# Optimization experiments

Measured on AMD Instinct MI355X. Metric: run time of the kernel, lower is better.

Reference implementation:

```python
import jax, jax.numpy as jnp
import numpy as np

B, S, H = 16, 4096, 768
N_SENT = 32
HH = H // 2  # per-direction LSTM hidden
NUM_LAYERS = 2


def attn_pool(x, mask, Wp, bp, v):
    # x: [N, L, H]; torch Linear is x @ W.T + b
    scores = jnp.einsum('nlh,h->nl', jnp.tanh(jnp.einsum('nlh,gh->nlg', x, Wp) + bp), v)
    if mask is not None:
        scores = jnp.where(mask, scores, -jnp.inf)
    w = jax.nn.softmax(scores, axis=1)  # [N, L]
    pooled = jnp.einsum('nlh,nl->nh', x, w)
    return pooled, w


def lstm_dir(x, Wih, Whh, bih, bhh, reverse):
    # x: [B, T, In]; PyTorch gate order i, f, g, o
    xg = jnp.einsum('bti,gi->btg', x, Wih) + bih  # [B, T, 4*HH]
    Bn = x.shape[0]
    init = (jnp.zeros((Bn, HH), x.dtype), jnp.zeros((Bn, HH), x.dtype))

    def step(carry, xt):
        h, c = carry
        g = xt + jnp.einsum('bh,gh->bg', h, Whh) + bhh
        i, f, gg, o = jnp.split(g, 4, axis=-1)
        c = jax.nn.sigmoid(f) * c + jax.nn.sigmoid(i) * jnp.tanh(gg)
        h = jax.nn.sigmoid(o) * jnp.tanh(c)
        return (h, c), h

    _, hs = jax.lax.scan(step, init, jnp.swapaxes(xg, 0, 1), reverse=reverse)
    return jnp.swapaxes(hs, 0, 1)  # [B, T, HH], time-aligned


def bilstm(x, Wih, Whh, bih, bhh):
    h = x
    for l in range(NUM_LAYERS):
        f = lstm_dir(h, Wih[l, 0], Whh[l, 0], bih[l, 0], bhh[l, 0], False)
        b = lstm_dir(h, Wih[l, 1], Whh[l, 1], bih[l, 1], bhh[l, 1], True)
        h = jnp.concatenate([f, b], axis=-1)  # [B, T, H]
    return h


def setup_inputs() -> dict:
    key = jax.random.key(0)
    ks = jax.random.split(key, 12)
    std = 0.02
    return {
        'hidden_states': jax.random.normal(ks[0], (B, S, H), jnp.float32),
        'attention_mask': jnp.ones((B, S), jnp.bool_),
        'w_proj_w': jax.random.normal(ks[1], (H, H), jnp.float32) * std,
        'w_proj_b': jnp.zeros((H,), jnp.float32),
        'w_vec': jax.random.normal(ks[2], (H,), jnp.float32) * std,
        'lstm_Wih': jax.random.normal(ks[3], (NUM_LAYERS, 2, 4 * HH, H), jnp.float32) * std,
        'lstm_Whh': jax.random.normal(ks[4], (NUM_LAYERS, 2, 4 * HH, HH), jnp.float32) * std,
        'lstm_bih': jnp.zeros((NUM_LAYERS, 2, 4 * HH), jnp.float32),
        'lstm_bhh': jnp.zeros((NUM_LAYERS, 2, 4 * HH), jnp.float32),
        's_proj_w': jax.random.normal(ks[5], (H, H), jnp.float32) * std,
        's_proj_b': jnp.zeros((H,), jnp.float32),
        's_vec': jax.random.normal(ks[6], (H,), jnp.float32) * std,
        'n_sent': N_SENT,
    }


def reference(hidden_states, attention_mask, w_proj_w, w_proj_b, w_vec,
              lstm_Wih, lstm_Whh, lstm_bih, lstm_bhh,
              s_proj_w, s_proj_b, s_vec, n_sent):
    b, s, h = hidden_states.shape
    L = s // n_sent
    # uniform sentence segmentation (boundaries at k*L-1): vectorized word attention
    x = hidden_states.reshape(b * n_sent, L, h)
    m = attention_mask.reshape(b * n_sent, L)
    pooled, w_attn = attn_pool(x, m, w_proj_w, w_proj_b, w_vec)  # [b*n_sent, h]
    sent = pooled.reshape(b, n_sent, h)
    enc = bilstm(sent, lstm_Wih, lstm_Whh, lstm_bih, lstm_bhh)  # [b, n_sent, h]
    doc, s_attn = attn_pool(enc, None, s_proj_w, s_proj_b, s_vec)  # [b, h]
    return doc, w_attn.reshape(b, n_sent, L), s_attn
```

## Files before the change

kernel.cpp:

```cpp
#include <hip/hip_runtime.h>
#include <math.h>

#define NB     16
#define NSENT  32
#define LW     128
#define HD     768
#define HH     384
#define NG     1536
#define NROWS  (NB*NSENT)
#define MW     (NROWS*LW)

typedef unsigned short ushort_t;
typedef unsigned long long u64;
typedef __attribute__((ext_vector_type(8))) short bf16x8;
typedef __attribute__((ext_vector_type(4))) float f32x4;
typedef __attribute__((ext_vector_type(4))) unsigned short u16x4;
typedef __attribute__((ext_vector_type(4))) unsigned int u32x4;

#define MFMA_BF16(a, b, c) __builtin_amdgcn_mfma_f32_16x16x32_bf16((a), (b), (c), 0, 0, 0)

__device__ __forceinline__ ushort_t f2bf(float x) {
  union { float f; unsigned u; } v; v.f = x;
  unsigned r = v.u + 0x7FFFu + ((v.u >> 16) & 1u);
  return (ushort_t)(r >> 16);
}
__device__ __forceinline__ float bf2f(ushort_t b) {
  union { unsigned u; float f; } v; v.u = ((unsigned)b) << 16; return v.f;
}
__device__ __forceinline__ float tanh_fast(float x) {
  float e = __builtin_amdgcn_exp2f(x * 2.88539008177793f);
  return 1.0f - 2.0f * __builtin_amdgcn_rcpf(e + 1.0f);
}
__device__ __forceinline__ float sigm(float x) {
  float e = __builtin_amdgcn_exp2f(-x * 1.44269504088896f);
  return __builtin_amdgcn_rcpf(1.0f + e);
}
__device__ __forceinline__ bf16x8 cvt8(float4 x, float4 y) {
  union { unsigned u[4]; bf16x8 v; } o;
  asm("v_cvt_pk_bf16_f32 %0, %1, %2" : "=v"(o.u[0]) : "v"(x.x), "v"(x.y));
  asm("v_cvt_pk_bf16_f32 %0, %1, %2" : "=v"(o.u[1]) : "v"(x.z), "v"(x.w));
  asm("v_cvt_pk_bf16_f32 %0, %1, %2" : "=v"(o.u[2]) : "v"(y.x), "v"(y.y));
  asm("v_cvt_pk_bf16_f32 %0, %1, %2" : "=v"(o.u[3]) : "v"(y.z), "v"(y.w));
  return o.v;
}
__device__ __forceinline__ void gload16(const void* g, void* l) {
  __builtin_amdgcn_global_load_lds(
      (const __attribute__((address_space(1))) unsigned int*)g,
      (__attribute__((address_space(3))) unsigned int*)l, 16, 0, 0);
}
__device__ __forceinline__ u64 ld64_ic(const u64* p) {
  return __hip_atomic_load(p, __ATOMIC_RELAXED, __HIP_MEMORY_SCOPE_AGENT);
}
__device__ __forceinline__ void st32_ic(unsigned* p, unsigned v) {
  __hip_atomic_store(p, v, __ATOMIC_RELAXED, __HIP_MEMORY_SCOPE_AGENT);
}
__device__ __forceinline__ bool bad64(u64 v) {
  return ((unsigned)v == 0xFFFFFFFFu) | ((unsigned)(v >> 32) == 0xFFFFFFFFu);
}

__global__ void cvt_kernel(const float* __restrict__ in, ushort_t* __restrict__ out, int n) {
  int i = blockIdx.x * blockDim.x + threadIdx.x;
  int st = gridDim.x * blockDim.x;
  for (; i < n; i += st) out[i] = f2bf(in[i]);
}

__global__ void cvtv_kernel(const float* __restrict__ in, ushort_t* __restrict__ out, int n8) {
  int i = blockIdx.x * blockDim.x + threadIdx.x;
  int st = gridDim.x * blockDim.x;
  for (; i < n8; i += st) {
    const float4* p = (const float4*)(in + (size_t)i * 8);
    float4 a = p[0], b = p[1];
    *(bf16x8*)(out + (size_t)i * 8) = cvt8(a, b);
  }
}

__global__ void addvec_kernel(const float* __restrict__ a, const float* __restrict__ b,
                              float* __restrict__ o, int n) {
  int i = blockIdx.x * blockDim.x + threadIdx.x;
  if (i < n) o[i] = a[i] + b[i];
}

__global__ void fillu_kernel(unsigned* __restrict__ p, unsigned v, int n) {
  int i = blockIdx.x * blockDim.x + threadIdx.x;
  int st = gridDim.x * blockDim.x;
  for (; i < n; i += st) p[i] = v;
}

template<int EPI, int SWZ>
__global__ __launch_bounds__(512, 2) void gemm_kernel(
    const ushort_t* __restrict__ Ab, const ushort_t* __restrict__ W,
    const float* __restrict__ bias, const float* __restrict__ vvec,
    float* __restrict__ outp, int Mtotal, int Ntot)
{
  __shared__ __align__(16) char smem[122880];
  short* Albuf = (short*)smem;
  short* Blbuf = (short*)(smem + 49152);
  float* pbuf  = (float*)smem;

  const int tid = threadIdx.x;
  int nc, m0;
  if constexpr (SWZ == 1) {
    const int g = blockIdx.x;
    const int x = g & 7, s = g >> 3;
    nc = s & 3;
    m0 = (x + 8 * (s >> 2)) * 128;
  } else {
    nc = blockIdx.x;
    m0 = blockIdx.y * 128;
  }
  const int n0 = nc * 192;

  const unsigned wbase = (unsigned)(tid & ~63) * 16;

  const int w = tid >> 6, wr = w >> 2, wc = w & 3;
  const int l = tid & 63, lm = l & 15, lg = l >> 4;
  int arow[4], ar7[4];
  #pragma unroll
  for (int mt = 0; mt < 4; ++mt) { arow[mt] = wr * 64 + mt * 16 + lm; ar7[mt] = arow[mt] & 7; }
  int brow[3], br7[3];
  #pragma unroll
  for (int nt = 0; nt < 3; ++nt) { brow[nt] = wc * 48 + nt * 16 + lm; br7[nt] = brow[nt] & 7; }

  f32x4 acc[4][3];
  #pragma unroll
  for (int mt = 0; mt < 4; ++mt)
    #pragma unroll
    for (int nt = 0; nt < 3; ++nt) acc[mt][nt] = (f32x4){0.f, 0.f, 0.f, 0.f};

  const int a0r = tid >> 3,          a0u = (tid & 7) ^ (a0r & 7);
  const int a1r = (tid + 512) >> 3,  a1u = (tid & 7) ^ (a1r & 7);
  const int b2r = (tid + 1024) >> 3, b2u = (tid & 7) ^ (b2r & 7);

  auto stage = [&](int buf, int s) {
    const int kc = s * 64;
    char* Ad = (char*)Albuf + buf * 16384;
    char* Bd = (char*)Blbuf + buf * 24576;
    gload16(Ab + (size_t)(m0 + a0r) * HD + kc + a0u * 8, Ad + wbase);
    gload16(Ab + (size_t)(m0 + a1r) * HD + kc + a1u * 8, Ad + 8192 + wbase);
    gload16(W + (size_t)(n0 + a0r) * HD + kc + a0u * 8, Bd + wbase);
    gload16(W + (size_t)(n0 + a1r) * HD + kc + a1u * 8, Bd + 8192 + wbase);
    gload16(W + (size_t)(n0 + b2r) * HD + kc + b2u * 8, Bd + 16384 + wbase);
  };
  auto compute = [&](int buf) {
    const short* Asrc = Albuf + buf * 8192;
    const short* Bsrc = Blbuf + buf * 12288;
    #pragma unroll
    for (int kk = 0; kk < 2; ++kk) {
      const int u = kk * 4 + lg;
      bf16x8 af[4], bfr[3];
      #pragma unroll
      for (int mt = 0; mt < 4; ++mt)
        af[mt] = *(const bf16x8*)((const char*)Asrc + (unsigned)((arow[mt] * 8 + (u ^ ar7[mt])) << 4));
      #pragma unroll
      for (int nt = 0; nt < 3; ++nt)
        bfr[nt] = *(const bf16x8*)((const char*)Bsrc + (unsigned)((brow[nt] * 8 + (u ^ br7[nt])) << 4));
      #pragma unroll
      for (int mt = 0; mt < 4; ++mt)
        #pragma unroll
        for (int nt = 0; nt < 3; ++nt)
          acc[mt][nt] = MFMA_BF16(af[mt], bfr[nt], acc[mt][nt]);
    }
  };

  stage(0, 0);
  stage(1, 1);
  #pragma unroll
  for (int s = 0; s < 12; ++s) {
    if (s + 2 < 12) stage((s + 2) % 3, s + 2);
    if (s <= 9)       asm volatile("s_waitcnt vmcnt(10)" ::: "memory");
    else if (s == 10) asm volatile("s_waitcnt vmcnt(5)" ::: "memory");
    else              asm volatile("s_waitcnt vmcnt(0)" ::: "memory");
    __builtin_amdgcn_sched_barrier(0);
    __builtin_amdgcn_s_barrier();
    __builtin_amdgcn_sched_barrier(0);
    compute(s % 3);
    __builtin_amdgcn_sched_barrier(0);
    __builtin_amdgcn_s_barrier();
  }

  if constexpr (EPI == 0) {
    float sp[16];
    #pragma unroll
    for (int e = 0; e < 16; ++e) sp[e] = 0.f;
    #pragma unroll
    for (int nt = 0; nt < 3; ++nt) {
      const int col = n0 + wc * 48 + nt * 16 + lm;
      const float bb = bias[col], vv = vvec[col];
      #pragma unroll
      for (int mt = 0; mt < 4; ++mt)
        #pragma unroll
        for (int r = 0; r < 4; ++r)
          sp[mt * 4 + r] += tanh_fast(acc[mt][nt][r] + bb) * vv;
    }
    #pragma unroll
    for (int msk = 1; msk < 16; msk <<= 1)
      #pragma unroll
      for (int e = 0; e < 16; ++e) sp[e] += __shfl_xor(sp[e], msk, 64);
    if (lm == 0) {
      #pragma unroll
      for (int mt = 0; mt < 4; ++mt)
        #pragma unroll
        for (int r = 0; r < 4; ++r)
          pbuf[(wr * 4 + wc) * 64 + mt * 16 + lg * 4 + r] = sp[mt * 4 + r];
    }
    __syncthreads();
    if (tid < 128) {
      const int wrr = tid >> 6, idx = tid & 63;
      float ssum = pbuf[(wrr * 4 + 0) * 64 + idx] + pbuf[(wrr * 4 + 1) * 64 + idx]
                 + pbuf[(wrr * 4 + 2) * 64 + idx] + pbuf[(wrr * 4 + 3) * 64 + idx];
      outp[(size_t)nc * Mtotal + m0 + wrr * 64 + idx] = ssum;
    }
  } else {
    #pragma unroll
    for (int nt = 0; nt < 3; ++nt) {
      const int col = n0 + wc * 48 + nt * 16 + lm;
      const float bb = bias[col];
      #pragma unroll
      for (int mt = 0; mt < 4; ++mt) {
        const int mrow = m0 + wr * 64 + mt * 16 + lg * 4;
        #pragma unroll
        for (int r = 0; r < 4; ++r)
          outp[(size_t)(mrow + r) * Ntot + col] = acc[mt][nt][r] + bb;
      }
    }
  }
}

__global__ __launch_bounds__(64) void softmax128_kernel(const float* __restrict__ sc,
                                                        float* __restrict__ wout) {
  const int row = blockIdx.x, lane = threadIdx.x;
  float a = sc[row * 128 + lane]          + sc[MW + row * 128 + lane]
          + sc[2 * MW + row * 128 + lane] + sc[3 * MW + row * 128 + lane];
  float b = sc[row * 128 + 64 + lane]          + sc[MW + row * 128 + 64 + lane]
          + sc[2 * MW + row * 128 + 64 + lane] + sc[3 * MW + row * 128 + 64 + lane];
  float mx = fmaxf(a, b);
  #pragma unroll
  for (int m = 1; m < 64; m <<= 1) mx = fmaxf(mx, __shfl_xor(mx, m, 64));
  float ea = __builtin_amdgcn_exp2f((a - mx) * 1.44269504088896f);
  float eb = __builtin_amdgcn_exp2f((b - mx) * 1.44269504088896f);
  float s = ea + eb;
  #pragma unroll
  for (int m = 1; m < 64; m <<= 1) s += __shfl_xor(s, m, 64);
  float inv = 1.0f / s;
  wout[row * 128 + lane] = ea * inv;
  wout[row * 128 + 64 + lane] = eb * inv;
}

__global__ __launch_bounds__(192) void pool_kernel(
    const ushort_t* __restrict__ xbf, const float* __restrict__ wattn,
    ushort_t* __restrict__ pooledbf)
{
  __shared__ float wl[128];
  const int n = blockIdx.x, tid = threadIdx.x;
  if (tid < 128) wl[tid] = wattn[n * 128 + tid];
  __syncthreads();
  const ushort_t* xb = xbf + (size_t)n * LW * HD + tid * 4;
  float a0 = 0, a1 = 0, a2 = 0, a3 = 0;
  float b0 = 0, b1 = 0, b2 = 0, b3 = 0;
  for (int lq = 0; lq < LW; lq += 2) {
    u16x4 v0 = *(const u16x4*)(xb + (size_t)lq * HD);
    u16x4 v1 = *(const u16x4*)(xb + (size_t)(lq + 1) * HD);
    float w0 = wl[lq], w1 = wl[lq + 1];
    a0 += w0 * bf2f(v0[0]); a1 += w0 * bf2f(v0[1]);
    a2 += w0 * bf2f(v0[2]); a3 += w0 * bf2f(v0[3]);
    b0 += w1 * bf2f(v1[0]); b1 += w1 * bf2f(v1[1]);
    b2 += w1 * bf2f(v1[2]); b3 += w1 * bf2f(v1[3]);
  }
  u16x4 o;
  o[0] = f2bf(a0 + b0); o[1] = f2bf(a1 + b1); o[2] = f2bf(a2 + b2); o[3] = f2bf(a3 + b3);
  *(u16x4*)(pooledbf + (size_t)n * HD + tid * 4) = o;
}

__global__ __launch_bounds__(384) void lstm_kernel(
    const ushort_t* __restrict__ whh_l,
    const float* __restrict__ xg,
    unsigned* __restrict__ hb32,
    ushort_t* __restrict__ encbf,
    float* __restrict__ encf,
    int writef32)
{
  __shared__ __align__(16) short h_lds[16 * HH];
  __shared__ float gatebuf[16][100];
  __shared__ float cst[16][24];
  const int tid = threadIdx.x;
  const int d = blockIdx.x >> 4, cid = blockIdx.x & 15;
  const int w = tid >> 6, l = tid & 63, lm = l & 15, lg = l >> 4;
  const int b = tid / 24, jj = tid % 24, gj = cid * 24 + jj;

  bf16x8 wf[12];
  {
    int r = w * 16 + lm;
    int qq = r / 24, jjr = r % 24;
    const ushort_t* src = whh_l + ((size_t)d * NG + qq * HH + cid * 24 + jjr) * HH + lg * 8;
    #pragma unroll
    for (int kk = 0; kk < 12; ++kk) wf[kk] = *(const bf16x8*)(src + kk * 32);
  }
  cst[b][jj] = 0.f;
  __syncthreads();

  const int hr = tid / 24, hc = tid % 24;
  const int hu = hc * 2, hx = hr & 7;

  for (int t = 0; t < NSENT; ++t) {
    const int trev = d ? (NSENT - 1 - t) : t;
    const float* xp = xg + (size_t)(b * NSENT + trev) * 3072 + d * NG + gj;
    float xi = xp[0], xf = xp[HH], xgg = xp[2 * HH], xo = xp[3 * HH];

    f32x4 acc = (f32x4){0.f, 0.f, 0.f, 0.f};
    if (t > 0) {
      const u64* src = (const u64*)hb32 + (size_t)(d * NSENT + (t - 1)) * 1536 + hr * 96 + hc * 4;
      u64 v0, v1, v2, v3;
      for (;;) {
        v0 = ld64_ic(src + 0); v1 = ld64_ic(src + 1);
        v2 = ld64_ic(src + 2); v3 = ld64_ic(src + 3);
        if (!(bad64(v0) | bad64(v1) | bad64(v2) | bad64(v3))) break;
        __builtin_amdgcn_s_sleep(1);
      }
      u32x4 lo = (u32x4){(unsigned)v0, (unsigned)(v0 >> 32), (unsigned)v1, (unsigned)(v1 >> 32)};
      u32x4 hi = (u32x4){(unsigned)v2, (unsigned)(v2 >> 32), (unsigned)v3, (unsigned)(v3 >> 32)};
      *(u32x4*)((char*)h_lds + (unsigned)((hr * 48 + ((hu    ) ^ hx)) * 16)) = lo;
      *(u32x4*)((char*)h_lds + (unsigned)((hr * 48 + ((hu + 1) ^ hx)) * 16)) = hi;
      __syncthreads();

      #pragma unroll
      for (int kk = 0; kk < 12; ++kk) {
        bf16x8 a = *(const bf16x8*)((char*)h_lds +
                      (unsigned)((lm * 48 + ((kk * 4 + lg) ^ (lm & 7))) * 16));
        acc = MFMA_BF16(a, wf[kk], acc);
      }
    }
    #pragma unroll
    for (int r = 0; r < 4; ++r)
      gatebuf[lg * 4 + r][w * 16 + lm] = acc[r];
    __syncthreads();

    {
      float gi = gatebuf[b][jj]      + xi;
      float gf = gatebuf[b][24 + jj] + xf;
      float gg = gatebuf[b][48 + jj] + xgg;
      float go = gatebuf[b][72 + jj] + xo;
      float c = sigm(gf) * cst[b][jj] + sigm(gi) * tanh_fast(gg);
      float h = sigm(go) * tanh_fast(c);
      cst[b][jj] = c;
      unsigned hv = (unsigned)f2bf(h);
      unsigned up = __shfl_down(hv, 1);
      if ((jj & 1) == 0 && t < NSENT - 1)
        st32_ic(hb32 + (size_t)(d * NSENT + t) * 3072 + b * 192 + gj / 2, hv | (up << 16));
      size_t eo = ((size_t)b * NSENT + trev) * HD + d * HH + gj;
      encbf[eo] = f2bf(h);
      if (writef32) encf[eo] = h;
    }
    __syncthreads();
  }
}

__global__ __launch_bounds__(64) void softmax32_kernel(const float* __restrict__ sc,
                                                       float* __restrict__ sattn,
                                                       float* __restrict__ sw) {
  const int b = blockIdx.x, lane = threadIdx.x;
  if (lane >= 32) return;
  float v = sc[b * 32 + lane]              + sc[NROWS + b * 32 + lane]
          + sc[2 * NROWS + b * 32 + lane]  + sc[3 * NROWS + b * 32 + lane];
  float mx = v;
  #pragma unroll
  for (int m = 1; m < 32; m <<= 1) mx = fmaxf(mx, __shfl_xor(mx, m, 32));
  float e = __builtin_amdgcn_exp2f((v - mx) * 1.44269504088896f);
  float s = e;
  #pragma unroll
  for (int m = 1; m < 32; m <<= 1) s += __shfl_xor(s, m, 32);
  float wv = e / s;
  sattn[b * 32 + lane] = wv;
  sw[b * 32 + lane] = wv;
}

__global__ __launch_bounds__(256) void doc_kernel(const float* __restrict__ enc2,
                                                  const float* __restrict__ sw,
                                                  float* __restrict__ doc) {
  __shared__ float wl[32];
  const int b = blockIdx.x, tid = threadIdx.x;
  if (tid < 32) wl[tid] = sw[b * 32 + tid];
  __syncthreads();
  for (int h = tid; h < HD; h += 256) {
    float a = 0.f;
    #pragma unroll
    for (int t = 0; t < 32; ++t) a += wl[t] * enc2[((size_t)b * 32 + t) * HD + h];
    doc[(size_t)b * HD + h] = a;
  }
}

extern "C" void kernel_launch(void* const* d_in, const int* in_sizes, int n_in,
                              void* d_out, int out_size, void* d_ws, size_t ws_size,
                              hipStream_t stream) {
  const float* hs  = (const float*)d_in[0];
  const float* wpw = (const float*)d_in[2];
  const float* wpb = (const float*)d_in[3];
  const float* wv  = (const float*)d_in[4];
  const float* Wih = (const float*)d_in[5];
  const float* Whh = (const float*)d_in[6];
  const float* bih = (const float*)d_in[7];
  const float* bhh = (const float*)d_in[8];
  const float* spw = (const float*)d_in[9];
  const float* spb = (const float*)d_in[10];
  const float* sv  = (const float*)d_in[11];

  float* out   = (float*)d_out;
  float* doc   = out;
  float* wattn = out + NB * HD;
  float* sattn = out + NB * HD + NROWS * LW;

  char* p = (char*)d_ws;
  auto take = [&p](size_t bytes) { char* q = p; p += (bytes + 255) & ~(size_t)255; return q; };
  ushort_t* wp_bf   = (ushort_t*)take((size_t)HD * HD * 2);
  ushort_t* sp_bf   = (ushort_t*)take((size_t)HD * HD * 2);
  ushort_t* wih_bf  = (ushort_t*)take((size_t)4 * NG * HD * 2);
  ushort_t* whh_bf  = (ushort_t*)take((size_t)4 * NG * HH * 2);
  float*    biasc   = (float*)take((size_t)4 * NG * 4);
  float*    wscore4 = (float*)take((size_t)4 * MW * 4);
  ushort_t* pooledbf= (ushort_t*)take((size_t)NROWS * HD * 2);
  float*    xgbuf   = (float*)take((size_t)NROWS * 2 * NG * 4);
  unsigned* hslots  = (unsigned*)take((size_t)2 * 2 * NSENT * 3072 * 4);
  ushort_t* enc1_bf = (ushort_t*)take((size_t)NROWS * HD * 2);
  ushort_t* enc2_bf = (ushort_t*)take((size_t)NROWS * HD * 2);
  float*    enc2    = (float*)take((size_t)NROWS * HD * 4);
  float*    sscore4 = (float*)take((size_t)4 * NROWS * 4);
  float*    sw      = (float*)take((size_t)NB * NSENT * 4);
  ushort_t* hs_bf   = (ushort_t*)take((size_t)MW * HD * 2);

  cvt_kernel<<<512, 256, 0, stream>>>(wpw, wp_bf, HD * HD);
  cvt_kernel<<<512, 256, 0, stream>>>(spw, sp_bf, HD * HD);
  cvt_kernel<<<2048, 256, 0, stream>>>(Wih, wih_bf, 4 * NG * HD);
  cvt_kernel<<<1024, 256, 0, stream>>>(Whh, whh_bf, 4 * NG * HH);
  addvec_kernel<<<24, 256, 0, stream>>>(bih, bhh, biasc, 4 * NG);
  fillu_kernel<<<768, 256, 0, stream>>>(hslots, 0xFFFFFFFFu, 2 * 2 * NSENT * 3072);
  cvtv_kernel<<<2048, 256, 0, stream>>>(hs, hs_bf, (int)((size_t)MW * HD / 8));

  gemm_kernel<0, 1><<<dim3(2048), 512, 0, stream>>>(
      hs_bf, wp_bf, wpb, wv, wscore4, MW, HD);
  softmax128_kernel<<<NROWS, 64, 0, stream>>>(wscore4, wattn);
  pool_kernel<<<NROWS, 192, 0, stream>>>(hs_bf, wattn, pooledbf);

  gemm_kernel<1, 0><<<dim3(16, NROWS / 128), 512, 0, stream>>>(
      pooledbf, wih_bf, biasc, nullptr, xgbuf, NROWS, 2 * NG);
  {
    const ushort_t* a0 = whh_bf; const float* a1 = xgbuf; unsigned* a2 = hslots;
    ushort_t* a3 = enc1_bf; float* a4 = enc2; int a5 = 0;
    void* args[] = { &a0, &a1, &a2, &a3, &a4, &a5 };
    hipLaunchCooperativeKernel((void*)lstm_kernel, dim3(32), dim3(384), args, 0, stream);
  }
  gemm_kernel<1, 0><<<dim3(16, NROWS / 128), 512, 0, stream>>>(
      enc1_bf, wih_bf + (size_t)2 * NG * HD, biasc + 2 * NG, nullptr,
      xgbuf, NROWS, 2 * NG);
  {
    const ushort_t* a0 = whh_bf + (size_t)2 * NG * HH; const float* a1 = xgbuf;
    unsigned* a2 = hslots + (size_t)2 * NSENT * 3072;
    ushort_t* a3 = enc2_bf; float* a4 = enc2; int a5 = 1;
    void* args[] = { &a0, &a1, &a2, &a3, &a4, &a5 };
    hipLaunchCooperativeKernel((void*)lstm_kernel, dim3(32), dim3(384), args, 0, stream);
  }

  gemm_kernel<0, 0><<<dim3(4, NROWS / 128), 512, 0, stream>>>(
      enc2_bf, sp_bf, spb, sv, sscore4, NROWS, HD);
  softmax32_kernel<<<NB, 64, 0, stream>>>(sscore4, sattn, sw);
  doc_kernel<<<NB, 256, 0, stream>>>(enc2, sw, doc);
}
```

Baseline: 393.9 us.

## Widen GEMM tile to 128x384 with K=32 stages and 4-deep buffering

The GEMM block tile grows from 128x192 to 128x384 columns, so each wave computes 4x6 MFMA tiles. The K step shrinks to 32 and the pipeline gets 4 buffers with 3 stages in flight, using a new swizzled LDS layout that packs two rows per 128-byte line. Each A tile is now reused across twice as many output columns, halving A global loads and the partial-score buffers (4 partials become 2), and the grids and softmax reductions are adjusted to match. The cost is more accumulator registers per thread, which with launch_bounds(512,2) may cause spills or lower occupancy, plus more barriers per K.

Measured after the change: 426.0 us. 1.08x slower.

```diff
diff --git a/kernel.cpp b/kernel.cpp
--- a/kernel.cpp
+++ b/kernel.cpp
@@ -92,9 +92,9 @@
     const float* __restrict__ bias, const float* __restrict__ vvec,
     float* __restrict__ outp, int Mtotal, int Ntot)
 {
-  __shared__ __align__(16) char smem[122880];
+  __shared__ __align__(16) char smem[131072];
   short* Albuf = (short*)smem;
-  short* Blbuf = (short*)(smem + 49152);
+  short* Blbuf = (short*)(smem + 32768);
   float* pbuf  = (float*)smem;
 
   const int tid = threadIdx.x;
@@ -102,78 +102,88 @@
   if constexpr (SWZ == 1) {
     const int g = blockIdx.x;
     const int x = g & 7, s = g >> 3;
-    nc = s & 3;
-    m0 = (x + 8 * (s >> 2)) * 128;
+    nc = s & 1;
+    m0 = (x + 8 * (s >> 1)) * 128;
   } else {
     nc = blockIdx.x;
     m0 = blockIdx.y * 128;
   }
-  const int n0 = nc * 192;
+  const int n0 = nc * 384;
 
   const unsigned wbase = (unsigned)(tid & ~63) * 16;
+
+  const int a_sr = tid >> 3, a_p = tid & 7;
+  const int a_l = a_p ^ (a_sr & 7);
+  const int a_row = 2 * a_sr + (a_l >> 2), a_k = (a_l & 3) * 8;
+  int b_row[3], b_k[3];
+  #pragma unroll
+  for (int i = 0; i < 3; ++i) {
+    int g = tid + 512 * i;
+    int sr = g >> 3, l = (g & 7) ^ (sr & 7);
+    b_row[i] = 2 * sr + (l >> 2); b_k[i] = (l & 3) * 8;
+  }
 
   const int w = tid >> 6, wr = w >> 2, wc = w & 3;
   const int l = tid & 63, lm = l & 15, lg = l >> 4;
-  int arow[4], ar7[4];
-  #pragma unroll
-  for (int mt = 0; mt < 4; ++mt) { arow[mt] = wr * 64 + mt * 16 + lm; ar7[mt] = arow[mt] & 7; }
-  int brow[3], br7[3];
-  #pragma unroll
-  for (int nt = 0; nt < 3; ++nt) { brow[nt] = wc * 48 + nt * 16 + lm; br7[nt] = brow[nt] & 7; }
-
-  f32x4 acc[4][3];
+  unsigned aoff[4];
+  #pragma unroll
+  for (int mt = 0; mt < 4; ++mt) {
+    int row = wr * 64 + mt * 16 + lm;
+    unsigned sr = (unsigned)(row >> 1), ul = (unsigned)(lg + 4 * (row & 1));
+    aoff[mt] = sr * 128 + ((ul ^ (sr & 7u)) << 4);
+  }
+  unsigned boff[6];
+  #pragma unroll
+  for (int nt = 0; nt < 6; ++nt) {
+    int row = wc * 96 + nt * 16 + lm;
+    unsigned sr = (unsigned)(row >> 1), ul = (unsigned)(lg + 4 * (row & 1));
+    boff[nt] = sr * 128 + ((ul ^ (sr & 7u)) << 4);
+  }
+
+  f32x4 acc[4][6];
   #pragma unroll
   for (int mt = 0; mt < 4; ++mt)
     #pragma unroll
-    for (int nt = 0; nt < 3; ++nt) acc[mt][nt] = (f32x4){0.f, 0.f, 0.f, 0.f};
-
-  const int a0r = tid >> 3,          a0u = (tid & 7) ^ (a0r & 7);
-  const int a1r = (tid + 512) >> 3,  a1u = (tid & 7) ^ (a1r & 7);
-  const int b2r = (tid + 1024) >> 3, b2u = (tid & 7) ^ (b2r & 7);
+    for (int nt = 0; nt < 6; ++nt) acc[mt][nt] = (f32x4){0.f, 0.f, 0.f, 0.f};
 
   auto stage = [&](int buf, int s) {
-    const int kc = s * 64;
-    char* Ad = (char*)Albuf + buf * 16384;
+    const int kc = s * 32;
+    char* Ad = (char*)Albuf + buf * 8192;
     char* Bd = (char*)Blbuf + buf * 24576;
-    gload16(Ab + (size_t)(m0 + a0r) * HD + kc + a0u * 8, Ad + wbase);
-    gload16(Ab + (size_t)(m0 + a1r) * HD + kc + a1u * 8, Ad + 8192 + wbase);
-    gload16(W + (size_t)(n0 + a0r) * HD + kc + a0u * 8, Bd + wbase);
-    gload16(W + (size_t)(n0 + a1r) * HD + kc + a1u * 8, Bd + 8192 + wbase);
-    gload16(W + (size_t)(n0 + b2r) * HD + kc + b2u * 8, Bd + 16384 + wbase);
+    gload16(Ab + (size_t)(m0 + a_row) * HD + kc + a_k, Ad + wbase);
+    gload16(W + (size_t)(n0 + b_row[0]) * HD + kc + b_k[0], Bd + wbase);
+    gload16(W + (size_t)(n0 + b_row[1]) * HD + kc + b_k[1], Bd + 8192 + wbase);
+    gload16(W + (size_t)(n0 + b_row[2]) * HD + kc + b_k[2], Bd + 16384 + wbase);
   };
   auto compute = [&](int buf) {
-    const short* Asrc = Albuf + buf * 8192;
-    const short* Bsrc = Blbuf + buf * 12288;
-    #pragma unroll
-    for (int kk = 0; kk < 2; ++kk) {
-      const int u = kk * 4 + lg;
-      bf16x8 af[4], bfr[3];
-      #pragma unroll
-      for (int mt = 0; mt < 4; ++mt)
-        af[mt] = *(const bf16x8*)((const char*)Asrc + (unsigned)((arow[mt] * 8 + (u ^ ar7[mt])) << 4));
-      #pragma unroll
-      for (int nt = 0; nt < 3; ++nt)
-        bfr[nt] = *(const bf16x8*)((const char*)Bsrc + (unsigned)((brow[nt] * 8 + (u ^ br7[nt])) << 4));
-      #pragma unroll
-      for (int mt = 0; mt < 4; ++mt)
-        #pragma unroll
-        for (int nt = 0; nt < 3; ++nt)
-          acc[mt][nt] = MFMA_BF16(af[mt], bfr[nt], acc[mt][nt]);
-    }
+    const char* Asrc = (const char*)Albuf + buf * 8192;
+    const char* Bsrc = (const char*)Blbuf + buf * 24576;
+    bf16x8 af[4], bfr[6];
+    #pragma unroll
+    for (int mt = 0; mt < 4; ++mt) af[mt] = *(const bf16x8*)(Asrc + aoff[mt]);
+    #pragma unroll
+    for (int nt = 0; nt < 6; ++nt) bfr[nt] = *(const bf16x8*)(Bsrc + boff[nt]);
+    #pragma unroll
+    for (int mt = 0; mt < 4; ++mt)
+      #pragma unroll
+      for (int nt = 0; nt < 6; ++nt)
+        acc[mt][nt] = MFMA_BF16(af[mt], bfr[nt], acc[mt][nt]);
   };
 
   stage(0, 0);
   stage(1, 1);
-  #pragma unroll
-  for (int s = 0; s < 12; ++s) {
-    if (s + 2 < 12) stage((s + 2) % 3, s + 2);
-    if (s <= 9)       asm volatile("s_waitcnt vmcnt(10)" ::: "memory");
-    else if (s == 10) asm volatile("s_waitcnt vmcnt(5)" ::: "memory");
+  stage(2, 2);
+  #pragma unroll
+  for (int s = 0; s < 24; ++s) {
+    if (s + 3 < 24) stage((s + 3) & 3, s + 3);
+    if (s <= 20)      asm volatile("s_waitcnt vmcnt(12)" ::: "memory");
+    else if (s == 21) asm volatile("s_waitcnt vmcnt(8)" ::: "memory");
+    else if (s == 22) asm volatile("s_waitcnt vmcnt(4)" ::: "memory");
     else              asm volatile("s_waitcnt vmcnt(0)" ::: "memory");
     __builtin_amdgcn_sched_barrier(0);
     __builtin_amdgcn_s_barrier();
     __builtin_amdgcn_sched_barrier(0);
-    compute(s % 3);
+    compute(s & 3);
     __builtin_amdgcn_sched_barrier(0);
     __builtin_amdgcn_s_barrier();
   }
@@ -183,8 +193,8 @@
     #pragma unroll
     for (int e = 0; e < 16; ++e) sp[e] = 0.f;
     #pragma unroll
-    for (int nt = 0; nt < 3; ++nt) {
-      const int col = n0 + wc * 48 + nt * 16 + lm;
+    for (int nt = 0; nt < 6; ++nt) {
+      const int col = n0 + wc * 96 + nt * 16 + lm;
       const float bb = bias[col], vv = vvec[col];
       #pragma unroll
       for (int mt = 0; mt < 4; ++mt)
@@ -212,8 +222,8 @@
     }
   } else {
     #pragma unroll
-    for (int nt = 0; nt < 3; ++nt) {
-      const int col = n0 + wc * 48 + nt * 16 + lm;
+    for (int nt = 0; nt < 6; ++nt) {
+      const int col = n0 + wc * 96 + nt * 16 + lm;
       const float bb = bias[col];
       #pragma unroll
       for (int mt = 0; mt < 4; ++mt) {
@@ -229,10 +239,8 @@
 __global__ __launch_bounds__(64) void softmax128_kernel(const float* __restrict__ sc,
                                                         float* __restrict__ wout) {
   const int row = blockIdx.x, lane = threadIdx.x;
-  float a = sc[row * 128 + lane]          + sc[MW + row * 128 + lane]
-          + sc[2 * MW + row * 128 + lane] + sc[3 * MW + row * 128 + lane];
-  float b = sc[row * 128 + 64 + lane]          + sc[MW + row * 128 + 64 + lane]
-          + sc[2 * MW + row * 128 + 64 + lane] + sc[3 * MW + row * 128 + 64 + lane];
+  float a = sc[row * 128 + lane]      + sc[MW + row * 128 + lane];
+  float b = sc[row * 128 + 64 + lane] + sc[MW + row * 128 + 64 + lane];
   float mx = fmaxf(a, b);
   #pragma unroll
   for (int m = 1; m < 64; m <<= 1) mx = fmaxf(mx, __shfl_xor(mx, m, 64));
@@ -359,8 +367,7 @@
                                                        float* __restrict__ sw) {
   const int b = blockIdx.x, lane = threadIdx.x;
   if (lane >= 32) return;
-  float v = sc[b * 32 + lane]              + sc[NROWS + b * 32 + lane]
-          + sc[2 * NROWS + b * 32 + lane]  + sc[3 * NROWS + b * 32 + lane];
+  float v = sc[b * 32 + lane] + sc[NROWS + b * 32 + lane];
   float mx = v;
   #pragma unroll
   for (int m = 1; m < 32; m <<= 1) mx = fmaxf(mx, __shfl_xor(mx, m, 32));
@@ -415,14 +422,14 @@
   ushort_t* wih_bf  = (ushort_t*)take((size_t)4 * NG * HD * 2);
   ushort_t* whh_bf  = (ushort_t*)take((size_t)4 * NG * HH * 2);
   float*    biasc   = (float*)take((size_t)4 * NG * 4);
-  float*    wscore4 = (float*)take((size_t)4 * MW * 4);
+  float*    wscore2 = (float*)take((size_t)2 * MW * 4);
   ushort_t* pooledbf= (ushort_t*)take((size_t)NROWS * HD * 2);
   float*    xgbuf   = (float*)take((size_t)NROWS * 2 * NG * 4);
   unsigned* hslots  = (unsigned*)take((size_t)2 * 2 * NSENT * 3072 * 4);
   ushort_t* enc1_bf = (ushort_t*)take((size_t)NROWS * HD * 2);
   ushort_t* enc2_bf = (ushort_t*)take((size_t)NROWS * HD * 2);
   float*    enc2    = (float*)take((size_t)NROWS * HD * 4);
-  float*    sscore4 = (float*)take((size_t)4 * NROWS * 4);
+  float*    sscore2 = (float*)take((size_t)2 * NROWS * 4);
   float*    sw      = (float*)take((size_t)NB * NSENT * 4);
   ushort_t* hs_bf   = (ushort_t*)take((size_t)MW * HD * 2);
 
@@ -434,12 +441,12 @@
   fillu_kernel<<<768, 256, 0, stream>>>(hslots, 0xFFFFFFFFu, 2 * 2 * NSENT * 3072);
   cvtv_kernel<<<2048, 256, 0, stream>>>(hs, hs_bf, (int)((size_t)MW * HD / 8));
 
-  gemm_kernel<0, 1><<<dim3(2048), 512, 0, stream>>>(
-      hs_bf, wp_bf, wpb, wv, wscore4, MW, HD);
-  softmax128_kernel<<<NROWS, 64, 0, stream>>>(wscore4, wattn);
+  gemm_kernel<0, 1><<<dim3(1024), 512, 0, stream>>>(
+      hs_bf, wp_bf, wpb, wv, wscore2, MW, HD);
+  softmax128_kernel<<<NROWS, 64, 0, stream>>>(wscore2, wattn);
   pool_kernel<<<NROWS, 192, 0, stream>>>(hs_bf, wattn, pooledbf);
 
-  gemm_kernel<1, 0><<<dim3(16, NROWS / 128), 512, 0, stream>>>(
+  gemm_kernel<1, 0><<<dim3(8, NROWS / 128), 512, 0, stream>>>(
       pooledbf, wih_bf, biasc, nullptr, xgbuf, NROWS, 2 * NG);
   {
     const ushort_t* a0 = whh_bf; const float* a1 = xgbuf; unsigned* a2 = hslots;
@@ -447,7 +454,7 @@
     void* args[] = { &a0, &a1, &a2, &a3, &a4, &a5 };
     hipLaunchCooperativeKernel((void*)lstm_kernel, dim3(32), dim3(384), args, 0, stream);
   }
-  gemm_kernel<1, 0><<<dim3(16, NROWS / 128), 512, 0, stream>>>(
+  gemm_kernel<1, 0><<<dim3(8, NROWS / 128), 512, 0, stream>>>(
       enc1_bf, wih_bf + (size_t)2 * NG * HD, biasc + 2 * NG, nullptr,
       xgbuf, NROWS, 2 * NG);
   {
@@ -458,8 +465,8 @@
     hipLaunchCooperativeKernel((void*)lstm_kernel, dim3(32), dim3(384), args, 0, stream);
   }
 
-  gemm_kernel<0, 0><<<dim3(4, NROWS / 128), 512, 0, stream>>>(
-      enc2_bf, sp_bf, spb, sv, sscore4, NROWS, HD);
-  softmax32_kernel<<<NB, 64, 0, stream>>>(sscore4, sattn, sw);
+  gemm_kernel<0, 0><<<dim3(2, NROWS / 128), 512, 0, stream>>>(
+      enc2_bf, sp_bf, spb, sv, sscore2, NROWS, HD);
+  softmax32_kernel<<<NB, 64, 0, stream>>>(sscore2, sattn, sw);
   doc_kernel<<<NB, 256, 0, stream>>>(enc2, sw, doc);
 }
```
